# Kernel optimization log

Hardware: AMD Instinct MI355X
Metric: run time of the kernel (lower is better)

## Reference

```python
import jax, jax.numpy as jnp
import numpy as np

B, T, C = 1, 4096, 1024
NH, NKV, HD = 16, 4, 64
N_REP = NH // NKV
WIN = 1024
EPS = 1e-5
ROPE_THETA = 10000.0


def setup_inputs() -> dict:
    key = jax.random.key(0)
    ks = jax.random.split(key, 6)
    s = 1.0 / np.sqrt(C)
    x = jax.random.normal(ks[0], (B, T, C), jnp.float32)
    wq = jax.random.normal(ks[1], (NH * HD, C), jnp.float32) * s
    wk = jax.random.normal(ks[2], (NKV * HD, C), jnp.float32) * s
    wv = jax.random.normal(ks[3], (NKV * HD, C), jnp.float32) * s
    wo = jax.random.normal(ks[4], (C, NH * HD), jnp.float32) * (1.0 / np.sqrt(NH * HD))
    q_norm_w = jnp.ones((HD,), jnp.float32)
    k_norm_w = jnp.ones((HD,), jnp.float32)
    # RoPE tables: (T, HD//2)
    inv_freq = 1.0 / (ROPE_THETA ** (np.arange(0, HD, 2, dtype=np.float32) / HD))
    ang = np.outer(np.arange(T, dtype=np.float32), inv_freq)
    freqs_cos = jnp.asarray(np.cos(ang), jnp.float32)
    freqs_sin = jnp.asarray(np.sin(ang), jnp.float32)
    return {"x": x, "wq": wq, "wk": wk, "wv": wv, "wo": wo,
            "q_norm_w": q_norm_w, "k_norm_w": k_norm_w,
            "freqs_cos": freqs_cos, "freqs_sin": freqs_sin}


def _rmsnorm(v, w):
    # RMSNorm over last dim (per-head)
    return v * jax.lax.rsqrt(jnp.mean(v * v, axis=-1, keepdims=True) + EPS) * w


def _rope(v, cos, sin):
    # v: (B, T, H, HD); interleaved complex rotation, matching torch polar freqs_cis
    vr, vi = v[..., 0::2], v[..., 1::2]
    c = cos[None, :, None, :]
    s = sin[None, :, None, :]
    out_r = vr * c - vi * s
    out_i = vr * s + vi * c
    return jnp.stack([out_r, out_i], axis=-1).reshape(v.shape)


def reference(x, wq, wk, wv, wo, q_norm_w, k_norm_w, freqs_cos, freqs_sin):
    xq = jnp.einsum('btc,dc->btd', x, wq).reshape(B, T, NH, HD)
    xk = jnp.einsum('btc,dc->btd', x, wk).reshape(B, T, NKV, HD)
    xv = jnp.einsum('btc,dc->btd', x, wv).reshape(B, T, NKV, HD)
    # per-head QK RMSNorm
    xq = _rmsnorm(xq, q_norm_w)
    xk = _rmsnorm(xk, k_norm_w)
    # RoPE
    xq = _rope(xq, freqs_cos, freqs_sin)
    xk = _rope(xk, freqs_cos, freqs_sin)
    # GQA: expand kv heads
    xk = jnp.repeat(xk, N_REP, axis=2)  # (B, T, NH, HD)
    xv = jnp.repeat(xv, N_REP, axis=2)
    scale = 1.0 / np.sqrt(HD)
    scores = jnp.einsum('bthd,bshd->bhts', xq, xk) * scale
    i = jnp.arange(T)[:, None]
    j = jnp.arange(T)[None, :]
    mask = (i >= j) & (i - j < WIN)  # causal + sliding window
    scores = jnp.where(mask[None, None], scores, -jnp.inf)
    attn = jax.nn.softmax(scores, axis=-1)
    y = jnp.einsum('bhts,bshd->bthd', attn, xv).reshape(B, T, NH * HD)
    return jnp.einsum('btd,cd->btc', y, wo)
```

## Files before the change

### kernel.cpp

```cpp
#include <hip/hip_runtime.h>
#include <hip/hip_bf16.h>


#define WIN_SZ 1024

typedef __attribute__((ext_vector_type(8))) short short8;
typedef __attribute__((ext_vector_type(8))) unsigned short ushort8;
typedef __attribute__((ext_vector_type(4))) float f32x4;
typedef __attribute__((ext_vector_type(16))) float f32x16;

#define GLOAD_LDS16(g, s)                                              \
  __builtin_amdgcn_global_load_lds(                                    \
      (const __attribute__((address_space(1))) unsigned int*)(g),      \
      (__attribute__((address_space(3))) unsigned int*)(s), 16, 0, 0)

__device__ __forceinline__ unsigned short f2bf(float f) {
  union { float f; unsigned u; } v; v.f = f;
  unsigned r = v.u + 0x7fffu + ((v.u >> 16) & 1u);
  return (unsigned short)(r >> 16);
}

__device__ __forceinline__ float bf2f(unsigned short b) {
  union { unsigned u; float f; } v; v.u = ((unsigned)b) << 16; return v.f;
}

__device__ __forceinline__ unsigned pk2bf(float lo, float hi) {
  __hip_bfloat162 h = __float22bfloat162_rn(make_float2(lo, hi));
  union { __hip_bfloat162 h; unsigned u; } c; c.h = h; return c.u;
}

__device__ __forceinline__ short8 frag4(unsigned w0, unsigned w1, unsigned w2, unsigned w3) {
  union { unsigned u[4]; short8 s; } x;
  x.u[0] = w0; x.u[1] = w1; x.u[2] = w2; x.u[3] = w3; return x.s;
}

__global__ __launch_bounds__(256) void k_f2b_all(const float* __restrict__ x,
                                                 const float* __restrict__ wq,
                                                 const float* __restrict__ wk,
                                                 const float* __restrict__ wv,
                                                 const float* __restrict__ wo,
                                                 unsigned short* __restrict__ xb,
                                                 unsigned short* __restrict__ wqkvb,
                                                 unsigned short* __restrict__ wob) {
  int q = blockIdx.x * 256 + threadIdx.x;
  const float* src;
  unsigned short* dst;
  int off;
  if (q < 1048576) { src = x; dst = xb; off = q; }
  else if (q < 1310720) { src = wq; dst = wqkvb; off = q - 1048576; }
  else if (q < 1376256) { src = wk; dst = wqkvb + 1024 * 1024; off = q - 1310720; }
  else if (q < 1441792) { src = wv; dst = wqkvb + 1280 * 1024; off = q - 1376256; }
  else { src = wo; dst = wob; off = q - 1441792; }
  float4 v = ((const float4*)src)[off];
  ushort4 o;
  o.x = f2bf(v.x); o.y = f2bf(v.y); o.z = f2bf(v.z); o.w = f2bf(v.w);
  ((ushort4*)dst)[off] = o;
}

template <int BF16OUT>
__global__ __launch_bounds__(256) void k_gemm16(const unsigned short* __restrict__ A,
                                                const unsigned short* __restrict__ B,
                                                void* __restrict__ Cv,
                                                int M, int N, int K) {
  __shared__ unsigned short As[128 * 64];
  __shared__ unsigned short Bs[128 * 64];
  const int tid = threadIdx.x;
  const int w = tid >> 6, l = tid & 63;
  const int wr = w >> 1, wc = w & 1;
  const int r = l & 15, g = l >> 4;
  const int m0 = blockIdx.y * 128, n0 = blockIdx.x * 128;
  const int lr = l >> 3, lc = l & 7;
  const int srowb = w * 32;

  f32x4 acc[4][4];
#pragma unroll
  for (int i = 0; i < 4; i++)
#pragma unroll
    for (int j = 0; j < 4; j++) acc[i][j] = {0.f, 0.f, 0.f, 0.f};

  const unsigned short* Ag = A + (size_t)(m0 + srowb + lr) * K + lc * 8;
  const unsigned short* Bg = B + (size_t)(n0 + srowb + lr) * K + lc * 8;

  for (int k0 = 0; k0 < K; k0 += 64) {
#pragma unroll
    for (int it = 0; it < 4; it++) {
      GLOAD_LDS16(Ag + (size_t)(it * 8) * K + k0, As + (srowb + it * 8) * 64);
      GLOAD_LDS16(Bg + (size_t)(it * 8) * K + k0, Bs + (srowb + it * 8) * 64);
    }
    __syncthreads();
#pragma unroll
    for (int kk = 0; kk < 2; kk++) {
      short8 af[4], bfr[4];
#pragma unroll
      for (int mi = 0; mi < 4; mi++)
        af[mi] = *(const short8*)((const char*)As + (wr * 64 + mi * 16 + r) * 128 + kk * 64 + g * 16);
#pragma unroll
      for (int nj = 0; nj < 4; nj++)
        bfr[nj] = *(const short8*)((const char*)Bs + (wc * 64 + nj * 16 + r) * 128 + kk * 64 + g * 16);
#pragma unroll
      for (int mi = 0; mi < 4; mi++)
#pragma unroll
        for (int nj = 0; nj < 4; nj++)
          acc[mi][nj] = __builtin_amdgcn_mfma_f32_16x16x32_bf16(af[mi], bfr[nj], acc[mi][nj], 0, 0, 0);
    }
    __syncthreads();
  }

#pragma unroll
  for (int mi = 0; mi < 4; mi++)
#pragma unroll
    for (int nj = 0; nj < 4; nj++) {
      int row = m0 + wr * 64 + mi * 16 + g * 4;
      int col = n0 + wc * 64 + nj * 16 + r;
      if (BF16OUT) {
        unsigned short* C = (unsigned short*)Cv;
#pragma unroll
        for (int e = 0; e < 4; e++)
          C[(size_t)(row + e) * N + col] = f2bf(acc[mi][nj][e]);
      } else {
        float* C = (float*)Cv;
#pragma unroll
        for (int e = 0; e < 4; e++)
          C[(size_t)(row + e) * N + col] = acc[mi][nj][e];
      }
    }
}

__global__ __launch_bounds__(256) void k_normrope(const unsigned short* __restrict__ QKV,
                                                  const float* __restrict__ qw,
                                                  const float* __restrict__ kw,
                                                  const float* __restrict__ fc,
                                                  const float* __restrict__ fs,
                                                  unsigned short* __restrict__ Qb,
                                                  unsigned short* __restrict__ Kb,
                                                  unsigned short* __restrict__ Vtg) {
  int gid = blockIdx.x * 4 + (threadIdx.x >> 6);
  int l = threadIdx.x & 63;
  int t = gid / 24;
  int u = gid - t * 24;
  if (u < 16) {
    float v = bf2f(QKV[(size_t)t * 1536 + u * 64 + l]);
    float ss = v * v;
#pragma unroll
    for (int off = 32; off; off >>= 1) ss += __shfl_xor(ss, off);
    float rms = rsqrtf(ss * (1.0f / 64.0f) + 1e-5f);
    float vn = v * rms * qw[l];
    float c = fc[t * 32 + (l >> 1)], s = fs[t * 32 + (l >> 1)];
    float p = __shfl_xor(vn, 1);
    float out = (l & 1) ? (p * s + vn * c) : (vn * c - p * s);
    Qb[(size_t)t * 1024 + u * 64 + l] = f2bf(out * 0.1803368801111204f);
  } else if (u < 20) {
    int hh = u - 16;
    float v = bf2f(QKV[(size_t)t * 1536 + 1024 + hh * 64 + l]);
    float ss = v * v;
#pragma unroll
    for (int off = 32; off; off >>= 1) ss += __shfl_xor(ss, off);
    float rms = rsqrtf(ss * (1.0f / 64.0f) + 1e-5f);
    float vn = v * rms * kw[l];
    float c = fc[t * 32 + (l >> 1)], s = fs[t * 32 + (l >> 1)];
    float p = __shfl_xor(vn, 1);
    float out = (l & 1) ? (p * s + vn * c) : (vn * c - p * s);
    Kb[(size_t)t * 256 + hh * 64 + l] = f2bf(out);
  } else {
    int hh = u - 20;
    Vtg[(size_t)(hh * 64 + l) * 4096 + t] = QKV[(size_t)t * 1536 + 1280 + hh * 64 + l];
  }
}

__global__ __launch_bounds__(512, 4) void k_attn4(const unsigned short* __restrict__ Qb,
                                                  const unsigned short* __restrict__ Kb,
                                                  const unsigned short* __restrict__ Vtg,
                                                  unsigned short* __restrict__ Yb) {
  __shared__ char smem[4 * 8192 + 1024];
  char* stage = smem;
  float* Obuf = (float*)smem;
  float* ml = (float*)(smem + 32768);

  const int hk = blockIdx.y;
  const int q0 = blockIdx.x * 32;
  const int tid = threadIdx.x, w = tid >> 6, l = tid & 63;
  const int hh = w & 3, half = w >> 2;
  const int h = hk * 4 + hh;
  const int l31 = l & 31, hi = l >> 5, l15 = l & 15;
  const int qrow = q0 + l31;

  int jlo = q0 - (WIN_SZ - 1);
  if (jlo < 0) jlo = 0;
  jlo &= ~63;
  const int jlast = ((q0 + 31) >> 6) << 6;
  const int nt = ((jlast - jlo) >> 6) + 1;
  const int nh0 = (nt + 1) >> 1;

  const int sb = tid >> 7;
  const int su = tid & 127;
  const int srow = su >> 1;
  const int sg = (su & 1) * 4;
  const int sbase = sb * 8192 + (srow & 31) * 256;
  const int srx = (srow & 15) << 4;
  const int srh = (srow >> 5) * 128;
  const bool isV = sb & 1;
  const unsigned short* gK = Kb + (size_t)srow * 256 + hk * 64 + sg * 8;
  const unsigned short* gV = Vtg + (size_t)(hk * 64 + srow) * 4096 + sg * 8;

  short8 qf[4];
#pragma unroll
  for (int ks = 0; ks < 4; ks++)
    qf[ks] = *(const short8*)(Qb + (size_t)qrow * 1024 + h * 64 + ks * 16 + hi * 8);

  f32x16 accO0, accO1;
#pragma unroll
  for (int i = 0; i < 16; i++) { accO0[i] = 0.f; accO1[i] = 0.f; }
  float m = -1e30f, lsum = 0.f;

  ushort8 pre[4];
  auto prefetch = [&](int s) {
    int jt0 = jlo + (s << 6);
    int t1 = nh0 + s;
    int jt1 = (t1 < nt) ? (jlo + (t1 << 6)) : jlo;
    int jt = (sb >= 2) ? jt1 : jt0;
    if (!isV) {
      const unsigned short* g = gK + (size_t)jt * 256;
#pragma unroll
      for (int e = 0; e < 4; e++) pre[e] = *(const ushort8*)(g + e * 8);
    } else {
      const unsigned short* g = gV + jt;
#pragma unroll
      for (int e = 0; e < 4; e++) pre[e] = *(const ushort8*)(g + e * 8);
    }
  };
  prefetch(0);

  const int kbase = half * 16384;
  const int vbase = kbase + 8192;

  for (int s = 0; s < nh0; ++s) {
    __syncthreads();
#pragma unroll
    for (int e = 0; e < 4; e++) {
      int dst = sbase + ((srh + (sg + e) * 16) ^ srx);
      *(ushort8*)(stage + dst) = pre[e];
    }
    __syncthreads();
    if (s + 1 < nh0) prefetch(s + 1);

    const int myt = half ? (nh0 + s) : s;
    if (myt < nt) {
      const int jt = jlo + (myt << 6);

      f32x16 st0, st1;
#pragma unroll
      for (int i = 0; i < 16; i++) { st0[i] = 0.f; st1[i] = 0.f; }
      __builtin_amdgcn_s_setprio(1);
#pragma unroll
      for (int ks = 0; ks < 4; ks++) {
        int colb = ks * 32 + hi * 16;
        short8 kf0 = *(const short8*)(stage + kbase + l31 * 256 + (colb ^ (l15 << 4)));
        st0 = __builtin_amdgcn_mfma_f32_32x32x16_bf16(kf0, qf[ks], st0, 0, 0, 0);
        short8 kf1 = *(const short8*)(stage + kbase + l31 * 256 + ((128 + colb) ^ (l15 << 4)));
        st1 = __builtin_amdgcn_mfma_f32_32x32x16_bf16(kf1, qf[ks], st1, 0, 0, 0);
      }
      __builtin_amdgcn_s_setprio(0);

      if (jt + 63 > q0 || (q0 + 31) - jt >= WIN_SZ) {
        const int jb = jt + hi * 4;
#pragma unroll
        for (int rg = 0; rg < 16; rg++) {
          int j0 = jb + (rg & 3) + 8 * (rg >> 2);
          if (!((j0 <= qrow) && (qrow - j0 < WIN_SZ))) st0[rg] = -3.0e38f;
          int j1 = j0 + 32;
          if (!((j1 <= qrow) && (qrow - j1 < WIN_SZ))) st1[rg] = -3.0e38f;
        }
      }

      float mx = st0[0];
#pragma unroll
      for (int rg = 1; rg < 16; rg++) mx = fmaxf(mx, st0[rg]);
#pragma unroll
      for (int rg = 0; rg < 16; rg++) mx = fmaxf(mx, st1[rg]);
      mx = fmaxf(mx, __shfl_xor(mx, 32));
      if (!__all(mx <= m + 8.0f)) {
        float mnew = fmaxf(m, mx);
        float alpha = exp2f(m - mnew);
#pragma unroll
        for (int rg = 0; rg < 16; rg++) { accO0[rg] *= alpha; accO1[rg] *= alpha; }
        lsum *= alpha;
        m = mnew;
      }
      float ps = 0.f;
#pragma unroll
      for (int rg = 0; rg < 16; rg++) { st0[rg] = exp2f(st0[rg] - m); ps += st0[rg]; }
#pragma unroll
      for (int rg = 0; rg < 16; rg++) { st1[rg] = exp2f(st1[rg] - m); ps += st1[rg]; }
      lsum += ps;

      unsigned pd0[2][4], pd1[2][4];
#pragma unroll
      for (int b = 0; b < 4; b++) {
        pd0[0][b] = pk2bf(st0[4 * b], st0[4 * b + 1]);
        pd1[0][b] = pk2bf(st0[4 * b + 2], st0[4 * b + 3]);
        pd0[1][b] = pk2bf(st1[4 * b], st1[4 * b + 1]);
        pd1[1][b] = pk2bf(st1[4 * b + 2], st1[4 * b + 3]);
      }

      __builtin_amdgcn_s_setprio(1);
#pragma unroll
      for (int jj = 0; jj < 2; jj++) {
#pragma unroll
        for (int ks2 = 0; ks2 < 2; ks2++) {
          unsigned a0 = pd0[jj][2 * ks2], a1 = pd0[jj][2 * ks2 + 1];
          unsigned b0 = pd1[jj][2 * ks2], b1 = pd1[jj][2 * ks2 + 1];
          unsigned a0x = __shfl_xor(a0, 32), a1x = __shfl_xor(a1, 32);
          unsigned b0x = __shfl_xor(b0, 32), b1x = __shfl_xor(b1, 32);
          unsigned w0 = hi ? a1x : a0;
          unsigned w1 = hi ? b1x : b0;
          unsigned w2 = hi ? a1 : a0x;
          unsigned w3 = hi ? b1 : b0x;
          short8 pf = frag4(w0, w1, w2, w3);
          int colb2 = jj * 64 + ks2 * 32 + hi * 16;
          short8 vf0 = *(const short8*)(stage + vbase + l31 * 256 + (colb2 ^ (l15 << 4)));
          accO0 = __builtin_amdgcn_mfma_f32_32x32x16_bf16(vf0, pf, accO0, 0, 0, 0);
          short8 vf1 = *(const short8*)(stage + vbase + l31 * 256 + ((128 + colb2) ^ (l15 << 4)));
          accO1 = __builtin_amdgcn_mfma_f32_32x32x16_bf16(vf1, pf, accO1, 0, 0, 0);
        }
      }
      __builtin_amdgcn_s_setprio(0);
    }
  }

  lsum += __shfl_xor(lsum, 32);
  __syncthreads();
  if (half == 1) {
#pragma unroll
    for (int dd = 0; dd < 2; dd++) {
      const f32x16& a = dd ? accO1 : accO0;
#pragma unroll
      for (int rg = 0; rg < 16; rg++) {
        int d = dd * 32 + 8 * (rg >> 2) + 4 * hi + (rg & 3);
        Obuf[(hh * 64 + d) * 32 + l31] = a[rg];
      }
    }
    if (!hi) { ml[(hh * 2 + 0) * 32 + l31] = m; ml[(hh * 2 + 1) * 32 + l31] = lsum; }
  }
  __syncthreads();
  if (half == 0) {
    float m1 = ml[(hh * 2 + 0) * 32 + l31];
    float l1 = ml[(hh * 2 + 1) * 32 + l31];
    float ms = fmaxf(m, m1);
    float a0 = exp2f(m - ms), a1 = exp2f(m1 - ms);
    float inv = 1.0f / (lsum * a0 + l1 * a1);
    a0 *= inv; a1 *= inv;
#pragma unroll
    for (int dd = 0; dd < 2; dd++) {
      const f32x16& a = dd ? accO1 : accO0;
#pragma unroll
      for (int b = 0; b < 4; b++) {
        float o[4];
#pragma unroll
        for (int e = 0; e < 4; e++) {
          int d = dd * 32 + 8 * b + 4 * hi + e;
          o[e] = a[4 * b + e] * a0 + Obuf[(hh * 64 + d) * 32 + l31] * a1;
        }
        union { unsigned u[2]; ushort4 v; } ov;
        ov.u[0] = pk2bf(o[0], o[1]);
        ov.u[1] = pk2bf(o[2], o[3]);
        *(ushort4*)(Yb + (size_t)qrow * 1024 + h * 64 + dd * 32 + b * 8 + hi * 4) = ov.v;
      }
    }
  }
}

extern "C" void kernel_launch(void* const* d_in, const int* in_sizes, int n_in,
                              void* d_out, int out_size, void* d_ws, size_t ws_size,
                              hipStream_t stream) {
  const float* x = (const float*)d_in[0];
  const float* wq = (const float*)d_in[1];
  const float* wk = (const float*)d_in[2];
  const float* wv = (const float*)d_in[3];
  const float* wo = (const float*)d_in[4];
  const float* qw = (const float*)d_in[5];
  const float* kw = (const float*)d_in[6];
  const float* fc = (const float*)d_in[7];
  const float* fs = (const float*)d_in[8];
  float* out = (float*)d_out;

  char* p = (char*)d_ws;
  auto alloc = [&](size_t b) {
    char* q = p;
    p += (b + 255) & ~(size_t)255;
    return q;
  };
  unsigned short* xb = (unsigned short*)alloc((size_t)4096 * 1024 * 2);
  unsigned short* wqkvb = (unsigned short*)alloc((size_t)1536 * 1024 * 2);
  unsigned short* wob = (unsigned short*)alloc((size_t)1024 * 1024 * 2);
  unsigned short* QKVb = (unsigned short*)alloc((size_t)4096 * 1536 * 2);
  unsigned short* Qb = (unsigned short*)alloc((size_t)4096 * 1024 * 2);
  unsigned short* Kb = (unsigned short*)alloc((size_t)4096 * 256 * 2);
  unsigned short* Vtg = (unsigned short*)alloc((size_t)256 * 4096 * 2);
  unsigned short* Yb = (unsigned short*)alloc((size_t)4096 * 1024 * 2);

  k_f2b_all<<<6656, 256, 0, stream>>>(x, wq, wk, wv, wo, xb, wqkvb, wob);
  k_gemm16<1><<<dim3(12, 32), 256, 0, stream>>>(xb, wqkvb, QKVb, 4096, 1536, 1024);
  k_normrope<<<24576, 256, 0, stream>>>(QKVb, qw, kw, fc, fs, Qb, Kb, Vtg);
  k_attn4<<<dim3(128, 4), 512, 0, stream>>>(Qb, Kb, Vtg, Yb);
  k_gemm16<0><<<dim3(8, 32), 256, 0, stream>>>(Yb, wob, out, 4096, 1024, 1024);
}
```

Before: 124.0 us.

## Double-buffer GEMM LDS tiles and reorder attention blocks for load balance

The GEMM kernel now uses two LDS buffers and issues the global-to-LDS loads for the next K tile before computing on the current one. This hides global load latency behind the MFMA work. The attention launch becomes a 1D grid that pairs early and late query tiles, which have short and long windows, and spreads KV heads so each compute unit gets balanced work. The cost is doubled GEMM LDS use (64KB), which may lower occupancy, and a remapped block order.

```diff
diff --git a/kernel.cpp b/kernel.cpp
--- a/kernel.cpp
+++ b/kernel.cpp
@@ -58,12 +58,12 @@
 }
 
 template <int BF16OUT>
-__global__ __launch_bounds__(256) void k_gemm16(const unsigned short* __restrict__ A,
+__global__ __launch_bounds__(256) void k_gemm2p(const unsigned short* __restrict__ A,
                                                 const unsigned short* __restrict__ B,
                                                 void* __restrict__ Cv,
                                                 int M, int N, int K) {
-  __shared__ unsigned short As[128 * 64];
-  __shared__ unsigned short Bs[128 * 64];
+  __shared__ unsigned short As[2][128 * 64];
+  __shared__ unsigned short Bs[2][128 * 64];
   const int tid = threadIdx.x;
   const int w = tid >> 6, l = tid & 63;
   const int wr = w >> 1, wc = w & 1;
@@ -81,22 +81,31 @@
   const unsigned short* Ag = A + (size_t)(m0 + srowb + lr) * K + lc * 8;
   const unsigned short* Bg = B + (size_t)(n0 + srowb + lr) * K + lc * 8;
 
-  for (int k0 = 0; k0 < K; k0 += 64) {
+  auto stage = [&](int buf, int k0) {
 #pragma unroll
     for (int it = 0; it < 4; it++) {
-      GLOAD_LDS16(Ag + (size_t)(it * 8) * K + k0, As + (srowb + it * 8) * 64);
-      GLOAD_LDS16(Bg + (size_t)(it * 8) * K + k0, Bs + (srowb + it * 8) * 64);
-    }
-    __syncthreads();
+      GLOAD_LDS16(Ag + (size_t)(it * 8) * K + k0, &As[buf][(srowb + it * 8) * 64]);
+      GLOAD_LDS16(Bg + (size_t)(it * 8) * K + k0, &Bs[buf][(srowb + it * 8) * 64]);
+    }
+  };
+
+  stage(0, 0);
+  __syncthreads();
+  int cur = 0;
+  const int NT = K >> 6;
+  for (int t = 0; t < NT; ++t) {
+    if (t + 1 < NT) stage(cur ^ 1, (t + 1) << 6);
+    const char* Ab = (const char*)As[cur];
+    const char* Bb = (const char*)Bs[cur];
 #pragma unroll
     for (int kk = 0; kk < 2; kk++) {
       short8 af[4], bfr[4];
 #pragma unroll
       for (int mi = 0; mi < 4; mi++)
-        af[mi] = *(const short8*)((const char*)As + (wr * 64 + mi * 16 + r) * 128 + kk * 64 + g * 16);
+        af[mi] = *(const short8*)(Ab + (wr * 64 + mi * 16 + r) * 128 + kk * 64 + g * 16);
 #pragma unroll
       for (int nj = 0; nj < 4; nj++)
-        bfr[nj] = *(const short8*)((const char*)Bs + (wc * 64 + nj * 16 + r) * 128 + kk * 64 + g * 16);
+        bfr[nj] = *(const short8*)(Bb + (wc * 64 + nj * 16 + r) * 128 + kk * 64 + g * 16);
 #pragma unroll
       for (int mi = 0; mi < 4; mi++)
 #pragma unroll
@@ -104,6 +113,7 @@
           acc[mi][nj] = __builtin_amdgcn_mfma_f32_16x16x32_bf16(af[mi], bfr[nj], acc[mi][nj], 0, 0, 0);
     }
     __syncthreads();
+    cur ^= 1;
   }
 
 #pragma unroll
@@ -176,8 +186,13 @@
   float* Obuf = (float*)smem;
   float* ml = (float*)(smem + 32768);
 
-  const int hk = blockIdx.y;
-  const int q0 = blockIdx.x * 32;
+  const int id = blockIdx.x;
+  const int cupair = id & 255, sel = id >> 8;
+  int qi = cupair >> 1;
+  if (sel) qi = 127 - qi;
+  const int hk = (cupair & 1) * 2 + sel;
+  const int q0 = qi * 32;
+
   const int tid = threadIdx.x, w = tid >> 6, l = tid & 63;
   const int hh = w & 3, half = w >> 2;
   const int h = hk * 4 + hh;
@@ -399,8 +414,8 @@
   unsigned short* Yb = (unsigned short*)alloc((size_t)4096 * 1024 * 2);
 
   k_f2b_all<<<6656, 256, 0, stream>>>(x, wq, wk, wv, wo, xb, wqkvb, wob);
-  k_gemm16<1><<<dim3(12, 32), 256, 0, stream>>>(xb, wqkvb, QKVb, 4096, 1536, 1024);
+  k_gemm2p<1><<<dim3(12, 32), 256, 0, stream>>>(xb, wqkvb, QKVb, 4096, 1536, 1024);
   k_normrope<<<24576, 256, 0, stream>>>(QKVb, qw, kw, fc, fs, Qb, Kb, Vtg);
-  k_attn4<<<dim3(128, 4), 512, 0, stream>>>(Qb, Kb, Vtg, Yb);
-  k_gemm16<0><<<dim3(8, 32), 256, 0, stream>>>(Yb, wob, out, 4096, 1024, 1024);
-}
+  k_attn4<<<512, 512, 0, stream>>>(Qb, Kb, Vtg, Yb);
+  k_gemm2p<0><<<dim3(8, 32), 256, 0, stream>>>(Yb, wob, out, 4096, 1024, 1024);
+}
```

New measurement: 123.2 us. About the same (-0.6%).
